# Kernel tuning notes

Hardware: AMD Instinct MI355X
Metric: run time of the kernel (lower is better)

The kernel has to match this reference:

```python
import jax, jax.numpy as jnp
import numpy as np

PI = float(np.pi)
LN_EPS = 1e-5
COS_EPS = 1e-6

D_HIDDEN, N_HEADS, D_HEAD, D_MLP = 1024, 16, 64, 4096
B, T = 4, 2048


def _xavier(key, shape):
    # torch xavier_uniform on 3D tensor: fan_in = shape[1]*shape[2]? torch uses
    # fan_in = shape[1] * receptive_field(shape[2:]), fan_out = shape[0] * rf.
    rf = 1
    for s in shape[2:]:
        rf *= s
    fan_in, fan_out = shape[1] * rf, shape[0] * rf
    bound = float(np.sqrt(6.0 / (fan_in + fan_out)))
    return jax.random.uniform(key, shape, jnp.float32, -bound, bound)


def setup_inputs() -> dict:
    key = jax.random.key(0)
    ks = jax.random.split(key, 10)
    x = jax.random.normal(ks[0], (B, T, D_HIDDEN), jnp.float32)
    W_Q = _xavier(ks[1], (N_HEADS, D_HIDDEN, 1))
    W_K = _xavier(ks[2], (N_HEADS, D_HIDDEN, 1))
    W_V = _xavier(ks[3], (N_HEADS, D_HIDDEN, D_HEAD))
    W_O = _xavier(ks[4], (D_HIDDEN, D_HEAD, N_HEADS))
    ln1_w = jnp.ones((D_HIDDEN,), jnp.float32)
    ln1_b = jnp.zeros((D_HIDDEN,), jnp.float32)
    ln2_w = jnp.ones((D_HIDDEN,), jnp.float32)
    ln2_b = jnp.zeros((D_HIDDEN,), jnp.float32)
    s1 = 1.0 / np.sqrt(D_HIDDEN)
    s2 = 1.0 / np.sqrt(D_MLP)
    W1 = jax.random.uniform(ks[5], (D_HIDDEN, D_MLP), jnp.float32, -s1, s1)
    b1 = jax.random.uniform(ks[6], (D_MLP,), jnp.float32, -s1, s1)
    W2 = jax.random.uniform(ks[7], (D_MLP, D_HIDDEN), jnp.float32, -s2, s2)
    b2 = jax.random.uniform(ks[8], (D_HIDDEN,), jnp.float32, -s2, s2)
    return {"x": x, "W_Q": W_Q, "W_K": W_K, "W_V": W_V, "W_O": W_O,
            "ln1_w": ln1_w, "ln1_b": ln1_b, "ln2_w": ln2_w, "ln2_b": ln2_b,
            "W1": W1, "b1": b1, "W2": W2, "b2": b2}


def _layer_norm(x, w, b):
    mu = jnp.mean(x, axis=-1, keepdims=True)
    var = jnp.mean(jnp.square(x - mu), axis=-1, keepdims=True)
    return (x - mu) * jax.lax.rsqrt(var + LN_EPS) * w + b


def _cos_attention(y, W_Q, W_K, W_V, W_O):
    q = jnp.einsum('btd,idh->btih', y, W_Q)  # (B,T,H,1)
    k = jnp.einsum('btd,idh->btih', y, W_K)  # (B,T,H,1)
    V = jnp.einsum('btd,idh->btih', y, W_V)  # (B,T,H,Dh)
    # use_tanh branch
    q = jnp.tanh(q) * (PI / 4)
    k = jnp.tanh(k) * (PI / 4)
    cos_k, sin_k = jnp.cos(k), jnp.sin(k)
    cos_KV = jnp.cumsum(cos_k * V, axis=1)
    sin_KV = jnp.cumsum(sin_k * V, axis=1)
    cos_Q, sin_Q = jnp.cos(q), jnp.sin(q)
    heads = cos_Q * cos_KV + sin_Q * sin_KV  # (B,T,H,Dh)
    # epsilon branch: normalizing denominator
    cos_K = jnp.cumsum(cos_k, axis=1)
    sin_K = jnp.cumsum(sin_k, axis=1)
    denom = cos_Q * cos_K + sin_Q * sin_K + COS_EPS  # (B,T,H,1)
    heads = heads / denom
    return jnp.einsum('dhi,btih->btd', W_O, heads)


def reference(x, W_Q, W_K, W_V, W_O, ln1_w, ln1_b, ln2_w, ln2_b, W1, b1, W2, b2):
    y = _layer_norm(x, ln1_w, ln1_b)
    x = x + _cos_attention(y, W_Q, W_K, W_V, W_O)
    y = _layer_norm(x, ln2_w, ln2_b)
    mlp = jnp.dot(jax.nn.gelu(jnp.dot(y, W1) + b1), W2) + b2
    return x + mlp
```

## Files before the change

kernel.cpp:

```cpp
#include <hip/hip_runtime.h>
#include <hip/hip_bf16.h>
#include <stdint.h>

typedef unsigned short u16;
typedef __attribute__((ext_vector_type(4))) unsigned int u32x4;
typedef __attribute__((ext_vector_type(8))) __bf16 bfx8;
typedef __attribute__((ext_vector_type(4))) float f32x4;

#define PI_F 3.14159265358979323846f

__device__ __forceinline__ float bf2f(u16 u) {
    unsigned v = ((unsigned)u) << 16; float f; __builtin_memcpy(&f, &v, 4); return f;
}
__device__ __forceinline__ u16 f2bf(float f) {
    unsigned u; __builtin_memcpy(&u, &f, 4);
    unsigned r = (u + 0x7fffu + ((u >> 16) & 1u)) >> 16; return (u16)r;
}

__device__ __forceinline__ void glds16(const u16* g, const u16* l) {
    __builtin_amdgcn_global_load_lds(
        (const __attribute__((address_space(1))) unsigned int*)(unsigned long long)g,
        (__attribute__((address_space(3))) unsigned int*)(unsigned int)(unsigned long long)l,
        16, 0, 0);
}

__global__ __launch_bounds__(256)
void tconv_kernel(const float* __restrict__ in, u16* __restrict__ out,
                  int R, int C, long inBatch, long outBatch)
{
    __shared__ float tile[64][65];
    const int tx = threadIdx.x & 63;
    const int ty = threadIdx.x >> 6;
    const int bc = blockIdx.x * 64;
    const int br = blockIdx.y * 64;
    const float* ip = in + (long)blockIdx.z * inBatch;
    u16* op = out + (long)blockIdx.z * outBatch;

    #pragma unroll
    for (int rr = ty; rr < 64; rr += 4) {
        int r = br + rr, c = bc + tx;
        tile[rr][tx] = (r < R && c < C) ? ip[(long)r * C + c] : 0.f;
    }
    __syncthreads();
    #pragma unroll
    for (int rr = ty; rr < 64; rr += 4) {
        int oc = bc + rr;
        int orr = br + tx;
        if (oc < C && orr < R)
            op[(long)oc * R + orr] = f2bf(tile[tx][rr]);
    }
}

template<bool DO_QK>
__global__ __launch_bounds__(256)
void ln_kernel(const float* __restrict__ X, const float* __restrict__ w,
               const float* __restrict__ b, u16* __restrict__ Ybf,
               const float* __restrict__ WQ, const float* __restrict__ WK,
               float* __restrict__ cqA, float* __restrict__ sqA,
               float* __restrict__ ckA, float* __restrict__ skA)
{
    __shared__ float yrow[1024];
    __shared__ float wsum[4], wsq[4];
    const int row = blockIdx.x;
    const int tid = threadIdx.x;
    const int lane = tid & 63;
    const int wv = tid >> 6;

    const float4 xv = ((const float4*)(X + (long)row * 1024))[tid];
    float s  = xv.x + xv.y + xv.z + xv.w;
    float sq = xv.x*xv.x + xv.y*xv.y + xv.z*xv.z + xv.w*xv.w;
    #pragma unroll
    for (int off = 32; off; off >>= 1) {
        s  += __shfl_down(s, off);
        sq += __shfl_down(sq, off);
    }
    if (lane == 0) { wsum[wv] = s; wsq[wv] = sq; }
    __syncthreads();
    const float ts = wsum[0] + wsum[1] + wsum[2] + wsum[3];
    const float tq = wsq[0] + wsq[1] + wsq[2] + wsq[3];
    const float mean = ts * (1.f / 1024.f);
    const float var  = tq * (1.f / 1024.f) - mean * mean;
    const float rstd = rsqrtf(var + 1e-5f);

    const float4 wv4 = ((const float4*)w)[tid];
    const float4 bv4 = ((const float4*)b)[tid];
    const float y0 = (xv.x - mean) * rstd * wv4.x + bv4.x;
    const float y1 = (xv.y - mean) * rstd * wv4.y + bv4.y;
    const float y2 = (xv.z - mean) * rstd * wv4.z + bv4.z;
    const float y3 = (xv.w - mean) * rstd * wv4.w + bv4.w;

    uint2 p;
    p.x = (unsigned)f2bf(y0) | ((unsigned)f2bf(y1) << 16);
    p.y = (unsigned)f2bf(y2) | ((unsigned)f2bf(y3) << 16);
    ((uint2*)(Ybf + (long)row * 1024))[tid] = p;

    if (DO_QK) {
        yrow[tid*4+0] = y0; yrow[tid*4+1] = y1;
        yrow[tid*4+2] = y2; yrow[tid*4+3] = y3;
        __syncthreads();
        #pragma unroll
        for (int i = 0; i < 4; ++i) {
            const int h = wv * 4 + i;
            const float* wqp = WQ + (long)h * 1024;
            const float* wkp = WK + (long)h * 1024;
            float dq = 0.f, dk = 0.f;
            #pragma unroll
            for (int j = 0; j < 16; ++j) {
                const float yv = yrow[lane + 64*j];
                dq = fmaf(yv, wqp[lane + 64*j], dq);
                dk = fmaf(yv, wkp[lane + 64*j], dk);
            }
            #pragma unroll
            for (int off = 32; off; off >>= 1) {
                dq += __shfl_down(dq, off);
                dk += __shfl_down(dk, off);
            }
            if (lane == 0) {
                const float aq = tanhf(dq) * (PI_F * 0.25f);
                const float ak = tanhf(dk) * (PI_F * 0.25f);
                float sv, cv;
                const long o = (long)h * 8192 + row;
                __sincosf(aq, &sv, &cv); cqA[o] = cv; sqA[o] = sv;
                __sincosf(ak, &sv, &cv); ckA[o] = cv; skA[o] = sv;
            }
        }
    }
}

__global__ __launch_bounds__(512)
void scan_kernel(const u16* __restrict__ V,
                 const float* __restrict__ cqA, const float* __restrict__ sqA,
                 const float* __restrict__ ckA, const float* __restrict__ skA,
                 u16* __restrict__ H)
{
    __shared__ float totcV[8][64], totsV[8][64];
    __shared__ float totc[8], tots[8];
    const int b = blockIdx.x >> 4;
    const int h = blockIdx.x & 15;
    const int wv = threadIdx.x >> 6;
    const int lane = threadIdx.x & 63;
    const long rowbase = (long)b * 2048;
    const long qbase = (long)h * 8192 + rowbase;
    const int t0 = wv * 256;

    const u16* vp = V + (rowbase + t0) * 1024 + (long)h * 64 + lane;

    float tc = 0.f, ts = 0.f, kc = 0.f, ks = 0.f;
    #pragma unroll 4
    for (int tt = 0; tt < 256; ++tt) {
        const float ck = ckA[qbase + t0 + tt];
        const float sk = skA[qbase + t0 + tt];
        const float vx = bf2f(vp[(long)tt * 1024]);
        tc = fmaf(ck, vx, tc); ts = fmaf(sk, vx, ts);
        kc += ck; ks += sk;
    }
    totcV[wv][lane] = tc; totsV[wv][lane] = ts;
    if (lane == 0) { totc[wv] = kc; tots[wv] = ks; }
    __syncthreads();

    float carC = 0.f, carS = 0.f, carKc = 0.f, carKs = 0.f;
    for (int w2 = 0; w2 < wv; ++w2) {
        carC += totcV[w2][lane]; carS += totsV[w2][lane];
        carKc += totc[w2]; carKs += tots[w2];
    }

    float csum = carC, ssum = carS, kcs = carKc, kss = carKs;
    u16* outp = H + (rowbase + t0) * 1024 + (long)h * 64 + lane;
    #pragma unroll 4
    for (int tt = 0; tt < 256; ++tt) {
        const long qo = qbase + t0 + tt;
        const float ck = ckA[qo], sk = skA[qo];
        const float cq = cqA[qo], sq2 = sqA[qo];
        const float vx = bf2f(vp[(long)tt * 1024]);
        csum = fmaf(ck, vx, csum); ssum = fmaf(sk, vx, ssum);
        kcs += ck; kss += sk;
        const float denom = cq * kcs + sq2 * kss + 1e-6f;
        const float hv = (cq * csum + sq2 * ssum) / denom;
        outp[(long)tt * 1024] = f2bf(hv);
    }
}

template<int EPI, int BN>
__global__ __launch_bounds__(512, 2)
void gemm5(const u16* __restrict__ A, const u16* __restrict__ B,
           void* __restrict__ Cout, const float* __restrict__ res,
           const float* __restrict__ bias, int N, int K, int nx)
{
    constexpr int NFR = BN / 64;
    constexpr int BSTR = BN * 64;
    __shared__ u16 As[2 * 256 * 64];
    __shared__ u16 Bs[2 * BSTR];

    const int tid  = threadIdx.x;
    const int lane = tid & 63;
    const int wave = tid >> 6;
    const int wr = wave >> 2;
    const int wc = wave & 3;
    const int rr = lane & 15;
    const int kq = lane >> 4;

    const int L = blockIdx.x;
    const int xcd = L & 7;
    const int qq = L >> 3;
    const int brow = ((qq / nx) * 8 + xcd) * 256;
    const int bcol = (qq % nx) * BN;

    const int v = tid >> 3;
    const int chp = tid & 7;
    const int clog = (chp - (v & 7)) & 7;
    const u16* AgB = A + (long)(brow + v) * K + clog * 8;
    const int rowB = (BN == 256) ? (v + (v & 32)) : v;
    const u16* BgB = B + (long)(bcol + rowB) * K + clog * 8;
    const long K64 = (long)64 * K;

    const int ph0 = ((kq + (rr & 7)) & 7) * 16;
    const int ph1 = ((kq + 4 + (rr & 7)) & 7) * 16;
    const int arb = rr * 128;
    const int aq0 = wr * 8192;
    const int aq1 = (2 + wr) * 8192;
    const int bq0 = (wc >> 1) * 8192 + (wc & 1) * 4096;
    const int bq1 = (2 + (wc >> 1)) * 8192 + (wc & 1) * 4096;

    f32x4 acc[8][NFR];
    #pragma unroll
    for (int i = 0; i < 8; ++i)
        #pragma unroll
        for (int j = 0; j < NFR; ++j) acc[i][j] = (f32x4){0.f, 0.f, 0.f, 0.f};

    const int NT = K >> 6;
    const char* AsB = (const char*)As;
    const char* BsB = (const char*)Bs;

#define STAGE_A0(nb, kn) { glds16(AgB + (kn),             &As[(nb)*16384 + tid*8]); \
                           glds16(AgB + (kn) + 2*K64,     &As[(nb)*16384 + 4096 + tid*8]); }
#define STAGE_A1(nb, kn) { glds16(AgB + (kn) + K64,       &As[(nb)*16384 + 8192 + tid*8]); \
                           glds16(AgB + (kn) + 3*K64,     &As[(nb)*16384 + 12288 + tid*8]); }
#define STAGE_B0(nb, kn) { glds16(BgB + (kn),             &Bs[(nb)*16384 + tid*8]); \
                           glds16(BgB + (kn) + 2*K64,     &Bs[(nb)*16384 + 4096 + tid*8]); }
#define STAGE_B1(nb, kn) { glds16(BgB + (kn) + (K64>>1),  &Bs[(nb)*16384 + 8192 + tid*8]); \
                           glds16(BgB + (kn) + (K64>>1) + 2*K64, &Bs[(nb)*16384 + 12288 + tid*8]); }
#define STAGE_B128(nb, kn) { glds16(BgB + (kn),           &Bs[(nb)*8192 + tid*8]); \
                             glds16(BgB + (kn) + K64,     &Bs[(nb)*8192 + 4096 + tid*8]); }
#define BAR  asm volatile("s_barrier" ::: "memory")
#define LGKM0 asm volatile("s_waitcnt lgkmcnt(0)" ::: "memory")
#define SB __builtin_amdgcn_sched_barrier(0)

    if constexpr (BN == 256) {
        STAGE_A0(0, 0); STAGE_B0(0, 0); STAGE_B1(0, 0); STAGE_A1(0, 0);
    } else {
        STAGE_A0(0, 0); STAGE_B128(0, 0); STAGE_A1(0, 0);
    }
    asm volatile("s_waitcnt vmcnt(0)" ::: "memory");
    BAR;

    for (int t = 0; t < NT; ++t) {
        const int buf = t & 1, nb = buf ^ 1;
        const long kn = (long)((t + 1 < NT) ? (t + 1) : 0) * 64;
        const char* Ap = AsB + buf * 32768;
        const char* Bp = BsB + buf * (BSTR * 2);

        if constexpr (BN == 256) {
            bfx8 a0[8], a1[8], b0[4], b1[4];
            #pragma unroll
            for (int mi = 0; mi < 4; ++mi) {
                a0[mi*2+0] = *(const bfx8*)(Ap + aq0 + mi*2048 + arb + ph0);
                a0[mi*2+1] = *(const bfx8*)(Ap + aq0 + mi*2048 + arb + ph1);
            }
            #pragma unroll
            for (int nf = 0; nf < 2; ++nf) {
                b0[nf*2+0] = *(const bfx8*)(Bp + bq0 + nf*2048 + arb + ph0);
                b0[nf*2+1] = *(const bfx8*)(Bp + bq0 + nf*2048 + arb + ph1);
            }
            STAGE_A0(nb, kn);
            BAR; LGKM0; SB;
            __builtin_amdgcn_s_setprio(1);
            #pragma unroll
            for (int mi = 0; mi < 4; ++mi)
                #pragma unroll
                for (int nf = 0; nf < 2; ++nf) {
                    acc[mi][nf] = __builtin_amdgcn_mfma_f32_16x16x32_bf16(a0[mi*2+0], b0[nf*2+0], acc[mi][nf], 0, 0, 0);
                    acc[mi][nf] = __builtin_amdgcn_mfma_f32_16x16x32_bf16(a0[mi*2+1], b0[nf*2+1], acc[mi][nf], 0, 0, 0);
                }
            __builtin_amdgcn_s_setprio(0); SB;
            asm volatile("s_waitcnt vmcnt(4)" ::: "memory");
            BAR;
            #pragma unroll
            for (int nf = 0; nf < 2; ++nf) {
                b1[nf*2+0] = *(const bfx8*)(Bp + bq1 + nf*2048 + arb + ph0);
                b1[nf*2+1] = *(const bfx8*)(Bp + bq1 + nf*2048 + arb + ph1);
            }
            STAGE_B0(nb, kn);
            BAR; LGKM0; SB;
            __builtin_amdgcn_s_setprio(1);
            #pragma unroll
            for (int mi = 0; mi < 4; ++mi)
                #pragma unroll
                for (int nf = 0; nf < 2; ++nf) {
                    acc[mi][2+nf] = __builtin_amdgcn_mfma_f32_16x16x32_bf16(a0[mi*2+0], b1[nf*2+0], acc[mi][2+nf], 0, 0, 0);
                    acc[mi][2+nf] = __builtin_amdgcn_mfma_f32_16x16x32_bf16(a0[mi*2+1], b1[nf*2+1], acc[mi][2+nf], 0, 0, 0);
                }
            __builtin_amdgcn_s_setprio(0); SB;
            asm volatile("s_waitcnt vmcnt(4)" ::: "memory");
            BAR;
            #pragma unroll
            for (int mi = 0; mi < 4; ++mi) {
                a1[mi*2+0] = *(const bfx8*)(Ap + aq1 + mi*2048 + arb + ph0);
                a1[mi*2+1] = *(const bfx8*)(Ap + aq1 + mi*2048 + arb + ph1);
            }
            STAGE_B1(nb, kn);
            BAR; LGKM0; SB;
            __builtin_amdgcn_s_setprio(1);
            #pragma unroll
            for (int mi = 0; mi < 4; ++mi)
                #pragma unroll
                for (int nf = 0; nf < 2; ++nf) {
                    acc[4+mi][2+nf] = __builtin_amdgcn_mfma_f32_16x16x32_bf16(a1[mi*2+0], b1[nf*2+0], acc[4+mi][2+nf], 0, 0, 0);
                    acc[4+mi][2+nf] = __builtin_amdgcn_mfma_f32_16x16x32_bf16(a1[mi*2+1], b1[nf*2+1], acc[4+mi][2+nf], 0, 0, 0);
                }
            __builtin_amdgcn_s_setprio(0); SB;
            BAR;
            STAGE_A1(nb, kn);
            BAR; SB;
            __builtin_amdgcn_s_setprio(1);
            #pragma unroll
            for (int mi = 0; mi < 4; ++mi)
                #pragma unroll
                for (int nf = 0; nf < 2; ++nf) {
                    acc[4+mi][nf] = __builtin_amdgcn_mfma_f32_16x16x32_bf16(a1[mi*2+0], b0[nf*2+0], acc[4+mi][nf], 0, 0, 0);
                    acc[4+mi][nf] = __builtin_amdgcn_mfma_f32_16x16x32_bf16(a1[mi*2+1], b0[nf*2+1], acc[4+mi][nf], 0, 0, 0);
                }
            __builtin_amdgcn_s_setprio(0); SB;
            asm volatile("s_waitcnt vmcnt(4)" ::: "memory");
            BAR;
        } else {
            bfx8 a0[8], a1[8], bb[4];
            #pragma unroll
            for (int mi = 0; mi < 4; ++mi) {
                a0[mi*2+0] = *(const bfx8*)(Ap + aq0 + mi*2048 + arb + ph0);
                a0[mi*2+1] = *(const bfx8*)(Ap + aq0 + mi*2048 + arb + ph1);
            }
            #pragma unroll
            for (int nf = 0; nf < 2; ++nf) {
                bb[nf*2+0] = *(const bfx8*)(Bp + bq0 + nf*2048 + arb + ph0);
                bb[nf*2+1] = *(const bfx8*)(Bp + bq0 + nf*2048 + arb + ph1);
            }
            STAGE_A0(nb, kn); STAGE_B128(nb, kn);
            BAR; LGKM0; SB;
            __builtin_amdgcn_s_setprio(1);
            #pragma unroll
            for (int mi = 0; mi < 4; ++mi)
                #pragma unroll
                for (int nf = 0; nf < 2; ++nf) {
                    acc[mi][nf] = __builtin_amdgcn_mfma_f32_16x16x32_bf16(a0[mi*2+0], bb[nf*2+0], acc[mi][nf], 0, 0, 0);
                    acc[mi][nf] = __builtin_amdgcn_mfma_f32_16x16x32_bf16(a0[mi*2+1], bb[nf*2+1], acc[mi][nf], 0, 0, 0);
                }
            __builtin_amdgcn_s_setprio(0); SB;
            asm volatile("s_waitcnt vmcnt(4)" ::: "memory");
            BAR;
            #pragma unroll
            for (int mi = 0; mi < 4; ++mi) {
                a1[mi*2+0] = *(const bfx8*)(Ap + aq1 + mi*2048 + arb + ph0);
                a1[mi*2+1] = *(const bfx8*)(Ap + aq1 + mi*2048 + arb + ph1);
            }
            STAGE_A1(nb, kn);
            BAR; LGKM0; SB;
            __builtin_amdgcn_s_setprio(1);
            #pragma unroll
            for (int mi = 0; mi < 4; ++mi)
                #pragma unroll
                for (int nf = 0; nf < 2; ++nf) {
                    acc[4+mi][nf] = __builtin_amdgcn_mfma_f32_16x16x32_bf16(a1[mi*2+0], bb[nf*2+0], acc[4+mi][nf], 0, 0, 0);
                    acc[4+mi][nf] = __builtin_amdgcn_mfma_f32_16x16x32_bf16(a1[mi*2+1], bb[nf*2+1], acc[4+mi][nf], 0, 0, 0);
                }
            __builtin_amdgcn_s_setprio(0); SB;
            asm volatile("s_waitcnt vmcnt(2)" ::: "memory");
            BAR;
        }
    }
#undef STAGE_A0
#undef STAGE_A1
#undef STAGE_B0
#undef STAGE_B1
#undef STAGE_B128
#undef BAR
#undef LGKM0
#undef SB

    const int crow0 = brow + wr * 128 + kq * 4;
    const int ccol0 = bcol + wc * (BN / 4) + rr;
    #pragma unroll
    for (int mi = 0; mi < 8; ++mi) {
        #pragma unroll
        for (int ni = 0; ni < NFR; ++ni) {
            const int col = ccol0 + ni * 16;
            #pragma unroll
            for (int r = 0; r < 4; ++r) {
                const int row = crow0 + mi * 16 + r;
                const long idx = (long)row * N + col;
                const float vvv = acc[mi][ni][r];
                if (EPI == 0) {
                    ((u16*)Cout)[idx] = f2bf(vvv);
                } else if (EPI == 1) {
                    ((float*)Cout)[idx] = vvv + res[idx];
                } else if (EPI == 2) {
                    const float hh = vvv + bias[col];
                    const float z = 0.7978845608028654f * (hh + 0.044715f * hh * hh * hh);
                    const float e = __expf(2.f * z);
                    const float th = 1.f - 2.f / (e + 1.f);
                    ((u16*)Cout)[idx] = f2bf(0.5f * hh * (1.f + th));
                } else {
                    ((float*)Cout)[idx] = vvv + res[idx] + bias[col];
                }
            }
        }
    }
}

extern "C" void kernel_launch(void* const* d_in, const int* in_sizes, int n_in,
                              void* d_out, int out_size, void* d_ws, size_t ws_size,
                              hipStream_t stream)
{
    (void)in_sizes; (void)n_in; (void)out_size; (void)ws_size;
    const float* x    = (const float*)d_in[0];
    const float* WQ   = (const float*)d_in[1];
    const float* WK   = (const float*)d_in[2];
    const float* WV   = (const float*)d_in[3];
    const float* WO   = (const float*)d_in[4];
    const float* ln1w = (const float*)d_in[5];
    const float* ln1b = (const float*)d_in[6];
    const float* ln2w = (const float*)d_in[7];
    const float* ln2b = (const float*)d_in[8];
    const float* W1   = (const float*)d_in[9];
    const float* b1   = (const float*)d_in[10];
    const float* W2   = (const float*)d_in[11];
    const float* b2   = (const float*)d_in[12];
    float* out = (float*)d_out;

    char* ws = (char*)d_ws;
    u16*   Ybf  = (u16*)(ws + 0);
    u16*   Vbf  = (u16*)(ws + 16777216);
    u16*   Hbf  = (u16*)(ws + 33554432);
    float* X2   = (float*)(ws + 50331648);
    u16*   H1   = (u16*)(ws + 83886080);
    u16*   WVT  = (u16*)(ws + 150994944);
    u16*   WOT  = (u16*)(ws + 153092096);
    u16*   W1T  = (u16*)(ws + 155189248);
    u16*   W2T  = (u16*)(ws + 163577856);
    float* CQ   = (float*)(ws + 171966464);
    float* SQ   = (float*)(ws + 172490752);
    float* CK   = (float*)(ws + 173015040);
    float* SK   = (float*)(ws + 173539328);

    tconv_kernel<<<dim3(1, 16, 16), 256, 0, stream>>>(WV, WVT, 1024, 64, 1024L*64, 64L*1024);
    tconv_kernel<<<dim3(1, 1, 1024), 256, 0, stream>>>(WO, WOT, 64, 16, 1024L, 1024L);
    tconv_kernel<<<dim3(64, 16, 1), 256, 0, stream>>>(W1, W1T, 1024, 4096, 0L, 0L);
    tconv_kernel<<<dim3(16, 64, 1), 256, 0, stream>>>(W2, W2T, 4096, 1024, 0L, 0L);

    ln_kernel<true><<<8192, 256, 0, stream>>>(x, ln1w, ln1b, Ybf, WQ, WK, CQ, SQ, CK, SK);

    gemm5<0, 128><<<256, 512, 0, stream>>>(Ybf, WVT, Vbf, nullptr, nullptr, 1024, 1024, 8);

    scan_kernel<<<64, 512, 0, stream>>>(Vbf, CQ, SQ, CK, SK, Hbf);

    gemm5<1, 128><<<256, 512, 0, stream>>>(Hbf, WOT, X2, x, nullptr, 1024, 1024, 8);

    ln_kernel<false><<<8192, 256, 0, stream>>>(X2, ln2w, ln2b, Ybf,
                                               nullptr, nullptr, nullptr, nullptr, nullptr, nullptr);

    gemm5<2, 256><<<512, 512, 0, stream>>>(Ybf, W1T, H1, nullptr, b1, 4096, 1024, 16);

    gemm5<3, 128><<<256, 512, 0, stream>>>(H1, W2T, out, X2, b2, 1024, 4096, 8);
}
```

Baseline: 507.5 us.

## Restructure GEMM waves to own full-row column strips with larger per-wave accumulators

Replaces the 2x4 wave grid in the GEMM with a 1x8 layout: each wave covers all 256 tile rows and a narrow column strip, so it holds 16xNF accumulator fragments and reuses its B fragment across all row fragments. Staging of the next K-tile is split into per-64-row slices interleaved with the compute phases, and launch bounds are relaxed to one block per CU so the larger register footprint fits. The aim is fewer B LDS reads and simpler staging. In exchange, every wave now reads the whole A tile from LDS, register pressure and occupancy change, and the column-strip epilogue stores are narrower.

```diff
diff --git a/kernel.cpp b/kernel.cpp
--- a/kernel.cpp
+++ b/kernel.cpp
@@ -181,23 +181,21 @@
 }
 
 template<int EPI, int BN>
-__global__ __launch_bounds__(512, 2)
-void gemm5(const u16* __restrict__ A, const u16* __restrict__ B,
+__global__ __launch_bounds__(512, 1)
+void gemm6(const u16* __restrict__ A, const u16* __restrict__ B,
            void* __restrict__ Cout, const float* __restrict__ res,
            const float* __restrict__ bias, int N, int K, int nx)
 {
-    constexpr int NFR = BN / 64;
-    constexpr int BSTR = BN * 64;
+    constexpr int NF = BN / 128;
+    constexpr int WC = BN / 8;
     __shared__ u16 As[2 * 256 * 64];
-    __shared__ u16 Bs[2 * BSTR];
+    __shared__ u16 Bs[2 * BN * 64];
 
     const int tid  = threadIdx.x;
     const int lane = tid & 63;
-    const int wave = tid >> 6;
-    const int wr = wave >> 2;
-    const int wc = wave & 3;
-    const int rr = lane & 15;
-    const int kq = lane >> 4;
+    const int w    = tid >> 6;
+    const int rr   = lane & 15;
+    const int kq   = lane >> 4;
 
     const int L = blockIdx.x;
     const int xcd = L & 7;
@@ -209,207 +207,177 @@
     const int chp = tid & 7;
     const int clog = (chp - (v & 7)) & 7;
     const u16* AgB = A + (long)(brow + v) * K + clog * 8;
-    const int rowB = (BN == 256) ? (v + (v & 32)) : v;
-    const u16* BgB = B + (long)(bcol + rowB) * K + clog * 8;
-    const long K64 = (long)64 * K;
+    const u16* BgB = B + (long)(bcol + v) * K + clog * 8;
 
     const int ph0 = ((kq + (rr & 7)) & 7) * 16;
     const int ph1 = ((kq + 4 + (rr & 7)) & 7) * 16;
     const int arb = rr * 128;
-    const int aq0 = wr * 8192;
-    const int aq1 = (2 + wr) * 8192;
-    const int bq0 = (wc >> 1) * 8192 + (wc & 1) * 4096;
-    const int bq1 = (2 + (wc >> 1)) * 8192 + (wc & 1) * 4096;
-
-    f32x4 acc[8][NFR];
+
+    f32x4 acc[16][NF];
     #pragma unroll
-    for (int i = 0; i < 8; ++i)
+    for (int i = 0; i < 16; ++i)
         #pragma unroll
-        for (int j = 0; j < NFR; ++j) acc[i][j] = (f32x4){0.f, 0.f, 0.f, 0.f};
+        for (int j = 0; j < NF; ++j) acc[i][j] = (f32x4){0.f, 0.f, 0.f, 0.f};
 
     const int NT = K >> 6;
-    const char* AsB = (const char*)As;
-    const char* BsB = (const char*)Bs;
-
-#define STAGE_A0(nb, kn) { glds16(AgB + (kn),             &As[(nb)*16384 + tid*8]); \
-                           glds16(AgB + (kn) + 2*K64,     &As[(nb)*16384 + 4096 + tid*8]); }
-#define STAGE_A1(nb, kn) { glds16(AgB + (kn) + K64,       &As[(nb)*16384 + 8192 + tid*8]); \
-                           glds16(AgB + (kn) + 3*K64,     &As[(nb)*16384 + 12288 + tid*8]); }
-#define STAGE_B0(nb, kn) { glds16(BgB + (kn),             &Bs[(nb)*16384 + tid*8]); \
-                           glds16(BgB + (kn) + 2*K64,     &Bs[(nb)*16384 + 4096 + tid*8]); }
-#define STAGE_B1(nb, kn) { glds16(BgB + (kn) + (K64>>1),  &Bs[(nb)*16384 + 8192 + tid*8]); \
-                           glds16(BgB + (kn) + (K64>>1) + 2*K64, &Bs[(nb)*16384 + 12288 + tid*8]); }
-#define STAGE_B128(nb, kn) { glds16(BgB + (kn),           &Bs[(nb)*8192 + tid*8]); \
-                             glds16(BgB + (kn) + K64,     &Bs[(nb)*8192 + 4096 + tid*8]); }
-#define BAR  asm volatile("s_barrier" ::: "memory")
+
+#define SA(nb, kn, s)  glds16(AgB + (kn) + (long)(s) * 64 * K, &As[(nb) * 16384 + (s) * 4096 + tid * 8])
+#define SBG(nb, kn, s) glds16(BgB + (kn) + (long)(s) * 64 * K, &Bs[(nb) * (BN * 64) + (s) * 4096 + tid * 8])
+#define BAR   asm volatile("s_barrier" ::: "memory")
 #define LGKM0 asm volatile("s_waitcnt lgkmcnt(0)" ::: "memory")
-#define SB __builtin_amdgcn_sched_barrier(0)
-
-    if constexpr (BN == 256) {
-        STAGE_A0(0, 0); STAGE_B0(0, 0); STAGE_B1(0, 0); STAGE_A1(0, 0);
-    } else {
-        STAGE_A0(0, 0); STAGE_B128(0, 0); STAGE_A1(0, 0);
-    }
+#define VMC4  asm volatile("s_waitcnt vmcnt(4)" ::: "memory")
+#define VMC2  asm volatile("s_waitcnt vmcnt(2)" ::: "memory")
+#define SBR   __builtin_amdgcn_sched_barrier(0)
+
+    if constexpr (BN == 256) { SBG(0,0,0); SBG(0,0,1); SBG(0,0,2); SBG(0,0,3); }
+    else                     { SBG(0,0,0); SBG(0,0,1); }
+    SA(0,0,0); SA(0,0,1); SA(0,0,2); SA(0,0,3);
     asm volatile("s_waitcnt vmcnt(0)" ::: "memory");
     BAR;
 
     for (int t = 0; t < NT; ++t) {
-        const int buf = t & 1, nb = buf ^ 1;
+        const int cur = t & 1, nxt = cur ^ 1;
         const long kn = (long)((t + 1 < NT) ? (t + 1) : 0) * 64;
-        const char* Ap = AsB + buf * 32768;
-        const char* Bp = BsB + buf * (BSTR * 2);
+        const char* Ap = (const char*)As + cur * 32768;
+        const char* Bp = (const char*)Bs + cur * (BN * 128);
 
         if constexpr (BN == 256) {
-            bfx8 a0[8], a1[8], b0[4], b1[4];
-            #pragma unroll
-            for (int mi = 0; mi < 4; ++mi) {
-                a0[mi*2+0] = *(const bfx8*)(Ap + aq0 + mi*2048 + arb + ph0);
-                a0[mi*2+1] = *(const bfx8*)(Ap + aq0 + mi*2048 + arb + ph1);
-            }
+            bfx8 bF[4], aF[8];
             #pragma unroll
             for (int nf = 0; nf < 2; ++nf) {
-                b0[nf*2+0] = *(const bfx8*)(Bp + bq0 + nf*2048 + arb + ph0);
-                b0[nf*2+1] = *(const bfx8*)(Bp + bq0 + nf*2048 + arb + ph1);
-            }
-            STAGE_A0(nb, kn);
-            BAR; LGKM0; SB;
-            __builtin_amdgcn_s_setprio(1);
-            #pragma unroll
-            for (int mi = 0; mi < 4; ++mi)
+                bF[nf*2+0] = *(const bfx8*)(Bp + w*4096 + nf*2048 + arb + ph0);
+                bF[nf*2+1] = *(const bfx8*)(Bp + w*4096 + nf*2048 + arb + ph1);
+            }
+            #pragma unroll
+            for (int mf = 0; mf < 4; ++mf) {
+                aF[mf*2+0] = *(const bfx8*)(Ap + mf*2048 + arb + ph0);
+                aF[mf*2+1] = *(const bfx8*)(Ap + mf*2048 + arb + ph1);
+            }
+            SBG(nxt, kn, 0); SBG(nxt, kn, 1);
+            BAR; LGKM0; SBR;
+            __builtin_amdgcn_s_setprio(1);
+            #pragma unroll
+            for (int mf = 0; mf < 4; ++mf)
                 #pragma unroll
                 for (int nf = 0; nf < 2; ++nf) {
-                    acc[mi][nf] = __builtin_amdgcn_mfma_f32_16x16x32_bf16(a0[mi*2+0], b0[nf*2+0], acc[mi][nf], 0, 0, 0);
-                    acc[mi][nf] = __builtin_amdgcn_mfma_f32_16x16x32_bf16(a0[mi*2+1], b0[nf*2+1], acc[mi][nf], 0, 0, 0);
+                    acc[mf][nf] = __builtin_amdgcn_mfma_f32_16x16x32_bf16(aF[mf*2+0], bF[nf*2+0], acc[mf][nf], 0, 0, 0);
+                    acc[mf][nf] = __builtin_amdgcn_mfma_f32_16x16x32_bf16(aF[mf*2+1], bF[nf*2+1], acc[mf][nf], 0, 0, 0);
                 }
-            __builtin_amdgcn_s_setprio(0); SB;
-            asm volatile("s_waitcnt vmcnt(4)" ::: "memory");
-            BAR;
-            #pragma unroll
-            for (int nf = 0; nf < 2; ++nf) {
-                b1[nf*2+0] = *(const bfx8*)(Bp + bq1 + nf*2048 + arb + ph0);
-                b1[nf*2+1] = *(const bfx8*)(Bp + bq1 + nf*2048 + arb + ph1);
-            }
-            STAGE_B0(nb, kn);
-            BAR; LGKM0; SB;
-            __builtin_amdgcn_s_setprio(1);
-            #pragma unroll
-            for (int mi = 0; mi < 4; ++mi)
+            __builtin_amdgcn_s_setprio(0); SBR; BAR;
+            #pragma unroll
+            for (int mf = 0; mf < 4; ++mf) {
+                aF[mf*2+0] = *(const bfx8*)(Ap + 8192 + mf*2048 + arb + ph0);
+                aF[mf*2+1] = *(const bfx8*)(Ap + 8192 + mf*2048 + arb + ph1);
+            }
+            SBG(nxt, kn, 2); SBG(nxt, kn, 3);
+            BAR; LGKM0; SBR;
+            __builtin_amdgcn_s_setprio(1);
+            #pragma unroll
+            for (int mf = 0; mf < 4; ++mf)
                 #pragma unroll
                 for (int nf = 0; nf < 2; ++nf) {
-                    acc[mi][2+nf] = __builtin_amdgcn_mfma_f32_16x16x32_bf16(a0[mi*2+0], b1[nf*2+0], acc[mi][2+nf], 0, 0, 0);
-                    acc[mi][2+nf] = __builtin_amdgcn_mfma_f32_16x16x32_bf16(a0[mi*2+1], b1[nf*2+1], acc[mi][2+nf], 0, 0, 0);
+                    acc[4+mf][nf] = __builtin_amdgcn_mfma_f32_16x16x32_bf16(aF[mf*2+0], bF[nf*2+0], acc[4+mf][nf], 0, 0, 0);
+                    acc[4+mf][nf] = __builtin_amdgcn_mfma_f32_16x16x32_bf16(aF[mf*2+1], bF[nf*2+1], acc[4+mf][nf], 0, 0, 0);
                 }
-            __builtin_amdgcn_s_setprio(0); SB;
-            asm volatile("s_waitcnt vmcnt(4)" ::: "memory");
-            BAR;
-            #pragma unroll
-            for (int mi = 0; mi < 4; ++mi) {
-                a1[mi*2+0] = *(const bfx8*)(Ap + aq1 + mi*2048 + arb + ph0);
-                a1[mi*2+1] = *(const bfx8*)(Ap + aq1 + mi*2048 + arb + ph1);
-            }
-            STAGE_B1(nb, kn);
-            BAR; LGKM0; SB;
-            __builtin_amdgcn_s_setprio(1);
-            #pragma unroll
-            for (int mi = 0; mi < 4; ++mi)
+            __builtin_amdgcn_s_setprio(0); SBR; VMC4; BAR;
+            #pragma unroll
+            for (int mf = 0; mf < 4; ++mf) {
+                aF[mf*2+0] = *(const bfx8*)(Ap + 16384 + mf*2048 + arb + ph0);
+                aF[mf*2+1] = *(const bfx8*)(Ap + 16384 + mf*2048 + arb + ph1);
+            }
+            SA(nxt, kn, 0); SA(nxt, kn, 1);
+            BAR; LGKM0; SBR;
+            __builtin_amdgcn_s_setprio(1);
+            #pragma unroll
+            for (int mf = 0; mf < 4; ++mf)
                 #pragma unroll
                 for (int nf = 0; nf < 2; ++nf) {
-                    acc[4+mi][2+nf] = __builtin_amdgcn_mfma_f32_16x16x32_bf16(a1[mi*2+0], b1[nf*2+0], acc[4+mi][2+nf], 0, 0, 0);
-                    acc[4+mi][2+nf] = __builtin_amdgcn_mfma_f32_16x16x32_bf16(a1[mi*2+1], b1[nf*2+1], acc[4+mi][2+nf], 0, 0, 0);
+                    acc[8+mf][nf] = __builtin_amdgcn_mfma_f32_16x16x32_bf16(aF[mf*2+0], bF[nf*2+0], acc[8+mf][nf], 0, 0, 0);
+                    acc[8+mf][nf] = __builtin_amdgcn_mfma_f32_16x16x32_bf16(aF[mf*2+1], bF[nf*2+1], acc[8+mf][nf], 0, 0, 0);
                 }
-            __builtin_amdgcn_s_setprio(0); SB;
-            BAR;
-            STAGE_A1(nb, kn);
-            BAR; SB;
-            __builtin_amdgcn_s_setprio(1);
-            #pragma unroll
-            for (int mi = 0; mi < 4; ++mi)
+            __builtin_amdgcn_s_setprio(0); SBR; BAR;
+            #pragma unroll
+            for (int mf = 0; mf < 4; ++mf) {
+                aF[mf*2+0] = *(const bfx8*)(Ap + 24576 + mf*2048 + arb + ph0);
+                aF[mf*2+1] = *(const bfx8*)(Ap + 24576 + mf*2048 + arb + ph1);
+            }
+            SA(nxt, kn, 2); SA(nxt, kn, 3);
+            BAR; LGKM0; SBR;
+            __builtin_amdgcn_s_setprio(1);
+            #pragma unroll
+            for (int mf = 0; mf < 4; ++mf)
                 #pragma unroll
                 for (int nf = 0; nf < 2; ++nf) {
-                    acc[4+mi][nf] = __builtin_amdgcn_mfma_f32_16x16x32_bf16(a1[mi*2+0], b0[nf*2+0], acc[4+mi][nf], 0, 0, 0);
-                    acc[4+mi][nf] = __builtin_amdgcn_mfma_f32_16x16x32_bf16(a1[mi*2+1], b0[nf*2+1], acc[4+mi][nf], 0, 0, 0);
+                    acc[12+mf][nf] = __builtin_amdgcn_mfma_f32_16x16x32_bf16(aF[mf*2+0], bF[nf*2+0], acc[12+mf][nf], 0, 0, 0);
+                    acc[12+mf][nf] = __builtin_amdgcn_mfma_f32_16x16x32_bf16(aF[mf*2+1], bF[nf*2+1], acc[12+mf][nf], 0, 0, 0);
                 }
-            __builtin_amdgcn_s_setprio(0); SB;
-            asm volatile("s_waitcnt vmcnt(4)" ::: "memory");
-            BAR;
+            __builtin_amdgcn_s_setprio(0); SBR; VMC2; BAR;
         } else {
-            bfx8 a0[8], a1[8], bb[4];
-            #pragma unroll
-            for (int mi = 0; mi < 4; ++mi) {
-                a0[mi*2+0] = *(const bfx8*)(Ap + aq0 + mi*2048 + arb + ph0);
-                a0[mi*2+1] = *(const bfx8*)(Ap + aq0 + mi*2048 + arb + ph1);
-            }
-            #pragma unroll
-            for (int nf = 0; nf < 2; ++nf) {
-                bb[nf*2+0] = *(const bfx8*)(Bp + bq0 + nf*2048 + arb + ph0);
-                bb[nf*2+1] = *(const bfx8*)(Bp + bq0 + nf*2048 + arb + ph1);
-            }
-            STAGE_A0(nb, kn); STAGE_B128(nb, kn);
-            BAR; LGKM0; SB;
-            __builtin_amdgcn_s_setprio(1);
-            #pragma unroll
-            for (int mi = 0; mi < 4; ++mi)
-                #pragma unroll
-                for (int nf = 0; nf < 2; ++nf) {
-                    acc[mi][nf] = __builtin_amdgcn_mfma_f32_16x16x32_bf16(a0[mi*2+0], bb[nf*2+0], acc[mi][nf], 0, 0, 0);
-                    acc[mi][nf] = __builtin_amdgcn_mfma_f32_16x16x32_bf16(a0[mi*2+1], bb[nf*2+1], acc[mi][nf], 0, 0, 0);
-                }
-            __builtin_amdgcn_s_setprio(0); SB;
-            asm volatile("s_waitcnt vmcnt(4)" ::: "memory");
-            BAR;
-            #pragma unroll
-            for (int mi = 0; mi < 4; ++mi) {
-                a1[mi*2+0] = *(const bfx8*)(Ap + aq1 + mi*2048 + arb + ph0);
-                a1[mi*2+1] = *(const bfx8*)(Ap + aq1 + mi*2048 + arb + ph1);
-            }
-            STAGE_A1(nb, kn);
-            BAR; LGKM0; SB;
-            __builtin_amdgcn_s_setprio(1);
-            #pragma unroll
-            for (int mi = 0; mi < 4; ++mi)
-                #pragma unroll
-                for (int nf = 0; nf < 2; ++nf) {
-                    acc[4+mi][nf] = __builtin_amdgcn_mfma_f32_16x16x32_bf16(a1[mi*2+0], bb[nf*2+0], acc[4+mi][nf], 0, 0, 0);
-                    acc[4+mi][nf] = __builtin_amdgcn_mfma_f32_16x16x32_bf16(a1[mi*2+1], bb[nf*2+1], acc[4+mi][nf], 0, 0, 0);
-                }
-            __builtin_amdgcn_s_setprio(0); SB;
-            asm volatile("s_waitcnt vmcnt(2)" ::: "memory");
-            BAR;
+            bfx8 bF[2], aF[16];
+            bF[0] = *(const bfx8*)(Bp + w*2048 + arb + ph0);
+            bF[1] = *(const bfx8*)(Bp + w*2048 + arb + ph1);
+            #pragma unroll
+            for (int mf = 0; mf < 8; ++mf) {
+                aF[mf*2+0] = *(const bfx8*)(Ap + mf*2048 + arb + ph0);
+                aF[mf*2+1] = *(const bfx8*)(Ap + mf*2048 + arb + ph1);
+            }
+            SBG(nxt, kn, 0); SBG(nxt, kn, 1); SA(nxt, kn, 0); SA(nxt, kn, 1);
+            BAR; LGKM0; SBR;
+            __builtin_amdgcn_s_setprio(1);
+            #pragma unroll
+            for (int mf = 0; mf < 8; ++mf) {
+                acc[mf][0] = __builtin_amdgcn_mfma_f32_16x16x32_bf16(aF[mf*2+0], bF[0], acc[mf][0], 0, 0, 0);
+                acc[mf][0] = __builtin_amdgcn_mfma_f32_16x16x32_bf16(aF[mf*2+1], bF[1], acc[mf][0], 0, 0, 0);
+            }
+            __builtin_amdgcn_s_setprio(0); SBR; VMC4; BAR;
+            #pragma unroll
+            for (int mf = 0; mf < 8; ++mf) {
+                aF[mf*2+0] = *(const bfx8*)(Ap + 16384 + mf*2048 + arb + ph0);
+                aF[mf*2+1] = *(const bfx8*)(Ap + 16384 + mf*2048 + arb + ph1);
+            }
+            SA(nxt, kn, 2); SA(nxt, kn, 3);
+            BAR; LGKM0; SBR;
+            __builtin_amdgcn_s_setprio(1);
+            #pragma unroll
+            for (int mf = 0; mf < 8; ++mf) {
+                acc[8+mf][0] = __builtin_amdgcn_mfma_f32_16x16x32_bf16(aF[mf*2+0], bF[0], acc[8+mf][0], 0, 0, 0);
+                acc[8+mf][0] = __builtin_amdgcn_mfma_f32_16x16x32_bf16(aF[mf*2+1], bF[1], acc[8+mf][0], 0, 0, 0);
+            }
+            __builtin_amdgcn_s_setprio(0); SBR; VMC2; BAR;
         }
     }
-#undef STAGE_A0
-#undef STAGE_A1
-#undef STAGE_B0
-#undef STAGE_B1
-#undef STAGE_B128
+    asm volatile("s_waitcnt vmcnt(0)" ::: "memory");
+
+#undef SA
+#undef SBG
 #undef BAR
 #undef LGKM0
-#undef SB
-
-    const int crow0 = brow + wr * 128 + kq * 4;
-    const int ccol0 = bcol + wc * (BN / 4) + rr;
+#undef VMC4
+#undef VMC2
+#undef SBR
+
     #pragma unroll
-    for (int mi = 0; mi < 8; ++mi) {
+    for (int ai = 0; ai < 16; ++ai) {
         #pragma unroll
-        for (int ni = 0; ni < NFR; ++ni) {
-            const int col = ccol0 + ni * 16;
+        for (int nf = 0; nf < NF; ++nf) {
+            const int col = bcol + w * WC + nf * 16 + rr;
             #pragma unroll
             for (int r = 0; r < 4; ++r) {
-                const int row = crow0 + mi * 16 + r;
+                const int row = brow + ai * 16 + kq * 4 + r;
                 const long idx = (long)row * N + col;
-                const float vvv = acc[mi][ni][r];
+                const float vv = acc[ai][nf][r];
                 if (EPI == 0) {
-                    ((u16*)Cout)[idx] = f2bf(vvv);
+                    ((u16*)Cout)[idx] = f2bf(vv);
                 } else if (EPI == 1) {
-                    ((float*)Cout)[idx] = vvv + res[idx];
+                    ((float*)Cout)[idx] = vv + res[idx];
                 } else if (EPI == 2) {
-                    const float hh = vvv + bias[col];
+                    const float hh = vv + bias[col];
                     const float z = 0.7978845608028654f * (hh + 0.044715f * hh * hh * hh);
                     const float e = __expf(2.f * z);
                     const float th = 1.f - 2.f / (e + 1.f);
                     ((u16*)Cout)[idx] = f2bf(0.5f * hh * (1.f + th));
                 } else {
-                    ((float*)Cout)[idx] = vvv + res[idx] + bias[col];
+                    ((float*)Cout)[idx] = vv + res[idx] + bias[col];
                 }
             }
         }
@@ -458,16 +426,16 @@
 
     ln_kernel<true><<<8192, 256, 0, stream>>>(x, ln1w, ln1b, Ybf, WQ, WK, CQ, SQ, CK, SK);
 
-    gemm5<0, 128><<<256, 512, 0, stream>>>(Ybf, WVT, Vbf, nullptr, nullptr, 1024, 1024, 8);
+    gemm6<0, 128><<<256, 512, 0, stream>>>(Ybf, WVT, Vbf, nullptr, nullptr, 1024, 1024, 8);
 
     scan_kernel<<<64, 512, 0, stream>>>(Vbf, CQ, SQ, CK, SK, Hbf);
 
-    gemm5<1, 128><<<256, 512, 0, stream>>>(Hbf, WOT, X2, x, nullptr, 1024, 1024, 8);
+    gemm6<1, 128><<<256, 512, 0, stream>>>(Hbf, WOT, X2, x, nullptr, 1024, 1024, 8);
 
     ln_kernel<false><<<8192, 256, 0, stream>>>(X2, ln2w, ln2b, Ybf,
                                                nullptr, nullptr, nullptr, nullptr, nullptr, nullptr);
 
-    gemm5<2, 256><<<512, 512, 0, stream>>>(Ybf, W1T, H1, nullptr, b1, 4096, 1024, 16);
-
-    gemm5<3, 128><<<256, 512, 0, stream>>>(H1, W2T, out, X2, b2, 1024, 4096, 8);
-}
+    gemm6<2, 256><<<512, 512, 0, stream>>>(Ybf, W1T, H1, nullptr, b1, 4096, 1024, 16);
+
+    gemm6<3, 128><<<256, 512, 0, stream>>>(H1, W2T, out, X2, b2, 1024, 4096, 8);
+}
```

New measurement: 510.9 us. Within noise of the previous version (+0.7%).
